# Performance work log

Hardware: AMD Instinct MI355X
Metric: run time of the kernel (lower is better)

## Reference

```python
import jax, jax.numpy as jnp
import numpy as np

N = 50000
E = 1600000
INDIM, HIDIM, OUTDIM = 256, 128, 64


def setup_inputs() -> dict:
    key = jax.random.key(0)
    ks = jax.random.split(key, 4)
    x = jax.random.normal(ks[0], (N, INDIM), dtype=jnp.float32)
    edge_index = jax.random.randint(ks[1], (2, E), 0, N, dtype=jnp.int32)
    W1 = jax.random.normal(ks[2], (INDIM, HIDIM), dtype=jnp.float32) / np.float32(np.sqrt(INDIM))
    b1 = jnp.zeros((HIDIM,), dtype=jnp.float32)
    W2 = jax.random.normal(ks[3], (HIDIM, OUTDIM), dtype=jnp.float32) / np.float32(np.sqrt(HIDIM))
    b2 = jnp.zeros((OUTDIM,), dtype=jnp.float32)
    return {"x": x, "edge_index": edge_index, "W1": W1, "b1": b1, "W2": W2, "b2": b2}


def _gcn_conv(x, row, col, norm, W, b):
    # PyG GCNConv: transform first, then normalized scatter-add aggregation, then bias
    h = x @ W                              # [N, out]
    msg = h[row] * norm[:, None]           # gather source features, scale by edge norm
    out = jax.ops.segment_sum(msg, col, num_segments=x.shape[0])  # scatter-add to dst
    return out + b


def reference(x, edge_index, W1, b1, W2, b2):
    n = x.shape[0]
    # add self loops (PyG default add_self_loops=True)
    loops = jnp.arange(n, dtype=edge_index.dtype)
    row = jnp.concatenate([edge_index[0], loops])  # source nodes
    col = jnp.concatenate([edge_index[1], loops])  # destination nodes
    # symmetric normalization: deg^{-1/2}[row] * deg^{-1/2}[col], deg over dst incl. self loops
    deg = jax.ops.segment_sum(jnp.ones_like(col, dtype=x.dtype), col, num_segments=n)
    dinv = jnp.where(deg > 0, jax.lax.rsqrt(jnp.maximum(deg, 1.0)), 0.0)
    norm = dinv[row] * dinv[col]
    h = jax.nn.relu(_gcn_conv(x, row, col, norm, W1, b1))
    return _gcn_conv(h, row, col, norm, W2, b2)
```

## Files before the change

### kernel.cpp

```cpp
#include <hip/hip_runtime.h>

#define NN 50000
#define NE 1600000
#define INDIM 256
#define HIDIM 128
#define OUTDIM 64

#define NRANGE 128
#define RSPAN 400
#define ACAP 16384
#define NBBLK 1563
#define NDEG 256

typedef unsigned int uint;
typedef unsigned long long ull;
typedef unsigned short ushort;
typedef __attribute__((ext_vector_type(8))) short bf16x8;
typedef __attribute__((ext_vector_type(4))) float f32x4;

__device__ __forceinline__ ushort f2bf(float f) {
    uint u = __float_as_uint(f);
    uint r = (u + 0x7FFFu + ((u >> 16) & 1u)) >> 16;
    return (ushort)r;
}
__device__ __forceinline__ uint pk2(float a, float b) {
    return (uint)f2bf(a) | ((uint)f2bf(b) << 16);
}
__device__ __forceinline__ float bf_lo(uint u) { return __uint_as_float(u << 16); }
__device__ __forceinline__ float bf_hi(uint u) { return __uint_as_float(u & 0xFFFF0000u); }

#define ACC8(u) do { \
    a0 += bf_lo((u).x); a1 += bf_hi((u).x); \
    a2 += bf_lo((u).y); a3 += bf_hi((u).y); \
    a4 += bf_lo((u).z); a5 += bf_hi((u).z); \
    a6 += bf_lo((u).w); a7 += bf_hi((u).w); \
} while (0)


__global__ void k_wt(const float* __restrict__ W1, const float* __restrict__ W2,
                     ushort* __restrict__ W1T, ushort* __restrict__ W2T) {
    int idx = blockIdx.x * 256 + threadIdx.x;
    if (idx < INDIM * HIDIM) {
        int k = idx / HIDIM, nn = idx % HIDIM;
        W1T[nn * INDIM + k] = f2bf(W1[idx]);
    } else {
        int j = idx - INDIM * HIDIM;
        if (j < HIDIM * OUTDIM) {
            int k = j / OUTDIM, nn = j % OUTDIM;
            W2T[nn * HIDIM + k] = f2bf(W2[j]);
        }
    }
}


__global__ void k_bcnt(const int* __restrict__ col, int* __restrict__ bcnt,
                       int* __restrict__ dhist) {
    __shared__ int bins[NRANGE];
    int tid = threadIdx.x;
    if (blockIdx.x == 0) dhist[tid] = 0;
    if (tid < NRANGE) bins[tid] = 0;
    __syncthreads();
    int base = blockIdx.x * 1024 + tid;
#pragma unroll
    for (int k = 0; k < 4; k++) {
        int i = base + k * 256;
        if (i < NE) atomicAdd(&bins[col[i] / RSPAN], 1);
    }
    __syncthreads();
    if (tid < NRANGE) bcnt[tid * NBBLK + blockIdx.x] = bins[tid];
}


__global__ void k_bscan(const int* __restrict__ bcnt, int* __restrict__ bbase,
                        int* __restrict__ rcur) {
    __shared__ int wsum[16];
    __shared__ int woff[16];
    int r = blockIdx.x;
    const int* src = bcnt + r * NBBLK;
    int* dst = bbase + r * NBBLK;
    int tid = threadIdx.x, lane = tid & 63, wid = tid >> 6;
    int seg = tid * 2;
    int l0 = (seg < NBBLK) ? src[seg] : 0;
    int l1 = (seg + 1 < NBBLK) ? src[seg + 1] : 0;
    int sum = l0 + l1;
    int incl = sum;
#pragma unroll
    for (int off = 1; off < 64; off <<= 1) {
        int t = __shfl_up(incl, off);
        if (lane >= off) incl += t;
    }
    if (lane == 63) wsum[wid] = incl;
    __syncthreads();
    if (wid == 0 && lane < 16) {
        int wv = wsum[lane];
        int wincl = wv;
#pragma unroll
        for (int off = 1; off < 16; off <<= 1) {
            int t = __shfl_up(wincl, off);
            if (lane >= off) wincl += t;
        }
        woff[lane] = wincl - wv;
    }
    __syncthreads();
    int run = incl - sum + woff[wid];
    if (seg < NBBLK) dst[seg] = run;
    if (seg + 1 < NBBLK) dst[seg + 1] = run + l0;
    if (tid == 1023) rcur[r] = run + sum;
}


__global__ void k_bscat(const int* __restrict__ row, const int* __restrict__ col,
                        const int* __restrict__ bbase, uint* __restrict__ staged) {
    __shared__ int cur[NRANGE];
    int tid = threadIdx.x;
    if (tid < NRANGE) cur[tid] = bbase[tid * NBBLK + blockIdx.x];
    __syncthreads();
    int base = blockIdx.x * 1024 + tid;
#pragma unroll
    for (int k = 0; k < 4; k++) {
        int i = base + k * 256;
        if (i < NE) {
            int d = col[i], s = row[i];
            int r = d / RSPAN;
            int off = atomicAdd(&cur[r], 1);
            staged[(size_t)r * ACAP + off] = ((uint)s << 10) | (uint)(d - r * RSPAN);
        }
    }
}


__global__ void k_sort(const uint* __restrict__ staged, const int* __restrict__ rcur,
                       int* __restrict__ row_ptr, float* __restrict__ dinv,
                       ushort* __restrict__ ssrc, int* __restrict__ dhist) {
    __shared__ int bins[RSPAN];
    __shared__ int wsum[16];
    __shared__ int woff[16];
    __shared__ int dh[NDEG];
    int r = blockIdx.x;
    int tid = threadIdx.x, lane = tid & 63, wid = tid >> 6;
    int lo = r * RSPAN;
    int count = rcur[r];
    int base = 0;
    for (int rr = 0; rr < r; rr++) base += rcur[rr];
    const uint* st = staged + (size_t)r * ACAP;

    if (tid < RSPAN) bins[tid] = 0;
    if (tid < NDEG) dh[tid] = 0;
    __syncthreads();

    for (int i = tid; i < count; i += 1024)
        atomicAdd(&bins[st[i] & 1023u], 1);
    __syncthreads();

    int v = (tid < RSPAN) ? bins[tid] : 0;
    int incl = v;
#pragma unroll
    for (int off = 1; off < 64; off <<= 1) {
        int t = __shfl_up(incl, off);
        if (lane >= off) incl += t;
    }
    if (lane == 63) wsum[wid] = incl;
    __syncthreads();
    if (wid == 0 && lane < 16) {
        int wv = wsum[lane];
        int wincl = wv;
#pragma unroll
        for (int off = 1; off < 16; off <<= 1) {
            int t = __shfl_up(wincl, off);
            if (lane >= off) wincl += t;
        }
        woff[lane] = wincl - wv;
    }
    __syncthreads();
    int excl = incl - v + woff[wid];
    int idx = lo + tid;
    if (tid < RSPAN && idx <= NN) {
        if (idx < NN) {
            row_ptr[idx] = base + excl;
            dinv[idx] = rsqrtf((float)(v + 1));
            atomicAdd(&dh[min(v, NDEG - 1)], 1);
        } else {
            row_ptr[NN] = base + excl;
        }
    }
    __syncthreads();
    if (tid < RSPAN) bins[tid] = base + excl;
    __syncthreads();
    if (tid < NDEG && dh[tid]) atomicAdd(&dhist[tid], dh[tid]);

    for (int i = tid; i < count; i += 1024) {
        uint rec = st[i];
        int pos = atomicAdd(&bins[rec & 1023u], 1);
        ssrc[pos] = (ushort)(rec >> 10);
    }
}


__global__ void k_dscan(const int* __restrict__ dhist, int* __restrict__ dstart,
                        int* __restrict__ dcur, int* __restrict__ ebase) {
    int lane = threadIdx.x;
    int b = lane * 4;
    int v0 = dhist[b], v1 = dhist[b + 1], v2 = dhist[b + 2], v3 = dhist[b + 3];
    int w0 = v0 * b, w1 = v1 * (b + 1), w2 = v2 * (b + 2), w3 = v3 * (b + 3);
    int s = v0 + v1 + v2 + v3;
    int sw = w0 + w1 + w2 + w3;
    int incl = s, inclw = sw;
#pragma unroll
    for (int off = 1; off < 64; off <<= 1) {
        int t = __shfl_up(incl, off);
        int t2 = __shfl_up(inclw, off);
        if (lane >= off) { incl += t; inclw += t2; }
    }
    int excl = incl - s, exclw = inclw - sw;
    dstart[b] = excl;            dcur[b] = excl;            ebase[b] = exclw;
    dstart[b + 1] = excl + v0;   dcur[b + 1] = excl + v0;   ebase[b + 1] = exclw + w0;
    dstart[b + 2] = excl + v0 + v1; dcur[b + 2] = excl + v0 + v1; ebase[b + 2] = exclw + w0 + w1;
    dstart[b + 3] = excl + v0 + v1 + v2; dcur[b + 3] = excl + v0 + v1 + v2; ebase[b + 3] = exclw + w0 + w1 + w2;
}


__global__ void k_dscat(const int* __restrict__ row_ptr, const float* __restrict__ dinv,
                        const int* __restrict__ dstart, int* __restrict__ dcur,
                        const int* __restrict__ ebase, int* __restrict__ perm,
                        int* __restrict__ row_ptr_p, float* __restrict__ dinv_p) {
    __shared__ int h[NDEG];
    __shared__ int boff[NDEG];
    int tid = threadIdx.x;
    int d = blockIdx.x * 256 + tid;
    h[tid] = 0;
    __syncthreads();
    int bin = 0, myoff = 0, deg = 0;
    if (d < NN) {
        deg = row_ptr[d + 1] - row_ptr[d];
        bin = min(deg, NDEG - 1);
        myoff = atomicAdd(&h[bin], 1);
    }
    __syncthreads();
    if (h[tid]) boff[tid] = atomicAdd(&dcur[tid], h[tid]);
    __syncthreads();
    if (d < NN) {
        int di = boff[bin] + myoff;
        perm[di] = d;
        int grank = di - dstart[bin];
        row_ptr_p[di] = ebase[bin] + grank * deg;
        dinv_p[di] = dinv[d];
    }
    if (d == 0) row_ptr_p[NN] = NE;
}


__global__ void k_csrperm(const int* __restrict__ perm, const int* __restrict__ row_ptr,
                          const int* __restrict__ row_ptr_p, const ushort* __restrict__ ssrc,
                          ushort* __restrict__ ssrc_p) {
    int g = blockIdx.x * 256 + threadIdx.x;
    int di = g >> 2, j = g & 3;
    if (di >= NN) return;
    int d = perm[di];
    int e0p = row_ptr_p[di];
    int deg = row_ptr_p[di + 1] - e0p;
    int e0 = row_ptr[d];
    for (int k = j; k < deg; k += 4)
        ssrc_p[e0p + k] = ssrc[e0 + k];
}


__global__ void k_gemm1(const float* __restrict__ A, const ushort* __restrict__ W1T,
                        const float* __restrict__ dinv, ushort* __restrict__ g1s, int n) {
    __shared__ ushort As[64 * 40];
    __shared__ ushort Bs[128 * 40];
    int tid = threadIdx.x;
    int w = tid >> 6, lane = tid & 63;
    int ln = lane & 15, quad = lane >> 4;
    int row0 = blockIdx.x * 64;
    int n0 = w * 32;

    f32x4 acc[4][2];
#pragma unroll
    for (int m = 0; m < 4; m++)
#pragma unroll
        for (int t = 0; t < 2; t++) acc[m][t] = (f32x4){0.f, 0.f, 0.f, 0.f};

    int ar = tid >> 2;
    int ac = (tid & 3) * 8;

    for (int k0 = 0; k0 < INDIM; k0 += 32) {
        {
            int gr = row0 + ar;
            uint4 u = make_uint4(0, 0, 0, 0);
            if (gr < n) {
                const float* p = A + (size_t)gr * INDIM + k0 + ac;
                float4 v0 = *(const float4*)p;
                float4 v1 = *(const float4*)(p + 4);
                u.x = pk2(v0.x, v0.y); u.y = pk2(v0.z, v0.w);
                u.z = pk2(v1.x, v1.y); u.w = pk2(v1.z, v1.w);
            }
            *(uint4*)(As + ar * 40 + ac) = u;
        }
#pragma unroll
        for (int it = 0; it < 2; it++) {
            int idx = tid + it * 256;
            int bn = idx >> 2, bc = (idx & 3) * 8;
            uint4 u = *(const uint4*)(W1T + (size_t)bn * INDIM + k0 + bc);
            *(uint4*)(Bs + bn * 40 + bc) = u;
        }
        __syncthreads();

        bf16x8 af[4], bf[2];
#pragma unroll
        for (int m = 0; m < 4; m++)
            af[m] = *(const bf16x8*)(As + (m * 16 + ln) * 40 + quad * 8);
#pragma unroll
        for (int t = 0; t < 2; t++)
            bf[t] = *(const bf16x8*)(Bs + (n0 + t * 16 + ln) * 40 + quad * 8);
#pragma unroll
        for (int m = 0; m < 4; m++)
#pragma unroll
            for (int t = 0; t < 2; t++)
                acc[m][t] = __builtin_amdgcn_mfma_f32_16x16x32_bf16(af[m], bf[t], acc[m][t], 0, 0, 0);
        __syncthreads();
    }

    int slice = w >> 1;
    int fbase = (w & 1) * 32;
#pragma unroll
    for (int m = 0; m < 4; m++) {
#pragma unroll
        for (int r = 0; r < 4; r++) {
            int gr = row0 + m * 16 + quad * 4 + r;
            if (gr < n) {
                float dv = dinv[gr];
#pragma unroll
                for (int t = 0; t < 2; t++) {
                    int cj = t * 16 + ln;
                    g1s[((size_t)slice * NN + gr) * 64 + fbase + cj] = f2bf(acc[m][t][r] * dv);
                }
            }
        }
    }
}


__global__ void k_agg1(const ushort* __restrict__ g1s, const float* __restrict__ dinv_p,
                       const int* __restrict__ row_ptr_p, const ushort* __restrict__ ssrc_p,
                       const int* __restrict__ perm, const float* __restrict__ b1,
                       ushort* __restrict__ hrb) {
    int slice = blockIdx.x & 1;
    int dbase = (blockIdx.x >> 1) * 32;
    int wid = threadIdx.x >> 6, lane = threadIdx.x & 63;
    int grp = lane >> 3, fl = lane & 7;
    int di = dbase + wid * 8 + grp;
    if (di >= NN) return;
    int d = perm[di];
    const ushort* gs = g1s + (size_t)slice * NN * 64 + fl * 8;
    float a0 = 0.f, a1 = 0.f, a2 = 0.f, a3 = 0.f;
    float a4 = 0.f, a5 = 0.f, a6 = 0.f, a7 = 0.f;
    int e0 = row_ptr_p[di], e1 = row_ptr_p[di + 1];
    if (e1 > e0) {
        int last = e1 - 1;
        int sB0 = ssrc_p[min(e0 + 0, last)];
        int sB1 = ssrc_p[min(e0 + 1, last)];
        int sB2 = ssrc_p[min(e0 + 2, last)];
        int sB3 = ssrc_p[min(e0 + 3, last)];
        uint4 uA0 = *(const uint4*)(gs + (size_t)sB0 * 64);
        uint4 uA1 = *(const uint4*)(gs + (size_t)sB1 * 64);
        uint4 uA2 = *(const uint4*)(gs + (size_t)sB2 * 64);
        uint4 uA3 = *(const uint4*)(gs + (size_t)sB3 * 64);
        sB0 = ssrc_p[min(e0 + 4, last)];
        sB1 = ssrc_p[min(e0 + 5, last)];
        sB2 = ssrc_p[min(e0 + 6, last)];
        sB3 = ssrc_p[min(e0 + 7, last)];
        for (int eb = e0; eb < e1; eb += 4) {
            int p0 = ssrc_p[min(eb + 8, last)];
            int p1 = ssrc_p[min(eb + 9, last)];
            int p2 = ssrc_p[min(eb + 10, last)];
            int p3 = ssrc_p[min(eb + 11, last)];
            uint4 v0 = *(const uint4*)(gs + (size_t)sB0 * 64);
            uint4 v1 = *(const uint4*)(gs + (size_t)sB1 * 64);
            uint4 v2 = *(const uint4*)(gs + (size_t)sB2 * 64);
            uint4 v3 = *(const uint4*)(gs + (size_t)sB3 * 64);
            uint4 z = make_uint4(0u, 0u, 0u, 0u);
            if (eb + 1 >= e1) uA1 = z;
            if (eb + 2 >= e1) uA2 = z;
            if (eb + 3 >= e1) uA3 = z;
            ACC8(uA0); ACC8(uA1); ACC8(uA2); ACC8(uA3);
            uA0 = v0; uA1 = v1; uA2 = v2; uA3 = v3;
            sB0 = p0; sB1 = p1; sB2 = p2; sB3 = p3;
        }
    }
    uint4 ud = *(const uint4*)(gs + (size_t)d * 64);
    ACC8(ud);
    float dv = dinv_p[di];
    const float* bp = b1 + slice * 64 + fl * 8;
    float4 bb0 = *(const float4*)bp;
    float4 bb1 = *(const float4*)(bp + 4);
    uint4 o;
    o.x = pk2(fmaxf(a0 * dv + bb0.x, 0.f), fmaxf(a1 * dv + bb0.y, 0.f));
    o.y = pk2(fmaxf(a2 * dv + bb0.z, 0.f), fmaxf(a3 * dv + bb0.w, 0.f));
    o.z = pk2(fmaxf(a4 * dv + bb1.x, 0.f), fmaxf(a5 * dv + bb1.y, 0.f));
    o.w = pk2(fmaxf(a6 * dv + bb1.z, 0.f), fmaxf(a7 * dv + bb1.w, 0.f));
    *(uint4*)(hrb + ((size_t)slice * NN + di) * 64 + fl * 8) = o;
}


__global__ void k_gemm2(const ushort* __restrict__ hrb, const ushort* __restrict__ W2T,
                        const float* __restrict__ dinv_p, const int* __restrict__ perm,
                        ushort* __restrict__ g2s, int n) {
    __shared__ ushort As[64 * 40];
    __shared__ ushort Bs[64 * 40];
    int tid = threadIdx.x;
    int w = tid >> 6, lane = tid & 63;
    int ln = lane & 15, quad = lane >> 4;
    int row0 = blockIdx.x * 64;
    int n0 = w * 16;

    f32x4 acc[4];
#pragma unroll
    for (int m = 0; m < 4; m++) acc[m] = (f32x4){0.f, 0.f, 0.f, 0.f};

    int ar = tid >> 2;
    int ac = (tid & 3) * 8;

    for (int k0 = 0; k0 < HIDIM; k0 += 32) {
        {
            int gr = row0 + ar;
            uint4 u = make_uint4(0, 0, 0, 0);
            if (gr < n) u = *(const uint4*)(hrb + ((size_t)(k0 >> 6) * NN + gr) * 64 + (k0 & 63) + ac);
            *(uint4*)(As + ar * 40 + ac) = u;
        }
        {
            int bn = tid >> 2, bc = (tid & 3) * 8;
            uint4 u = *(const uint4*)(W2T + (size_t)bn * HIDIM + k0 + bc);
            *(uint4*)(Bs + bn * 40 + bc) = u;
        }
        __syncthreads();

        bf16x8 bf = *(const bf16x8*)(Bs + (n0 + ln) * 40 + quad * 8);
#pragma unroll
        for (int m = 0; m < 4; m++) {
            bf16x8 af = *(const bf16x8*)(As + (m * 16 + ln) * 40 + quad * 8);
            acc[m] = __builtin_amdgcn_mfma_f32_16x16x32_bf16(af, bf, acc[m], 0, 0, 0);
        }
        __syncthreads();
    }

    int col = n0 + ln;
#pragma unroll
    for (int m = 0; m < 4; m++) {
#pragma unroll
        for (int r = 0; r < 4; r++) {
            int gr = row0 + m * 16 + quad * 4 + r;
            if (gr < n) {
                int gd = perm[gr];
                g2s[(size_t)gd * 64 + col] = f2bf(acc[m][r] * dinv_p[gr]);
            }
        }
    }
}


__global__ void k_agg2(const ushort* __restrict__ g2s, const float* __restrict__ dinv_p,
                       const int* __restrict__ row_ptr_p, const ushort* __restrict__ ssrc_p,
                       const int* __restrict__ perm, const float* __restrict__ b2,
                       float* __restrict__ out) {
    int dbase = blockIdx.x * 32;
    int wid = threadIdx.x >> 6, lane = threadIdx.x & 63;
    int grp = lane >> 3, fl = lane & 7;
    int di = dbase + wid * 8 + grp;
    if (di >= NN) return;
    int d = perm[di];
    const ushort* gs = g2s + fl * 8;
    float a0 = 0.f, a1 = 0.f, a2 = 0.f, a3 = 0.f;
    float a4 = 0.f, a5 = 0.f, a6 = 0.f, a7 = 0.f;
    int e0 = row_ptr_p[di], e1 = row_ptr_p[di + 1];
    if (e1 > e0) {
        int last = e1 - 1;
        int sB0 = ssrc_p[min(e0 + 0, last)];
        int sB1 = ssrc_p[min(e0 + 1, last)];
        int sB2 = ssrc_p[min(e0 + 2, last)];
        int sB3 = ssrc_p[min(e0 + 3, last)];
        uint4 uA0 = *(const uint4*)(gs + (size_t)sB0 * 64);
        uint4 uA1 = *(const uint4*)(gs + (size_t)sB1 * 64);
        uint4 uA2 = *(const uint4*)(gs + (size_t)sB2 * 64);
        uint4 uA3 = *(const uint4*)(gs + (size_t)sB3 * 64);
        sB0 = ssrc_p[min(e0 + 4, last)];
        sB1 = ssrc_p[min(e0 + 5, last)];
        sB2 = ssrc_p[min(e0 + 6, last)];
        sB3 = ssrc_p[min(e0 + 7, last)];
        for (int eb = e0; eb < e1; eb += 4) {
            int p0 = ssrc_p[min(eb + 8, last)];
            int p1 = ssrc_p[min(eb + 9, last)];
            int p2 = ssrc_p[min(eb + 10, last)];
            int p3 = ssrc_p[min(eb + 11, last)];
            uint4 v0 = *(const uint4*)(gs + (size_t)sB0 * 64);
            uint4 v1 = *(const uint4*)(gs + (size_t)sB1 * 64);
            uint4 v2 = *(const uint4*)(gs + (size_t)sB2 * 64);
            uint4 v3 = *(const uint4*)(gs + (size_t)sB3 * 64);
            uint4 z = make_uint4(0u, 0u, 0u, 0u);
            if (eb + 1 >= e1) uA1 = z;
            if (eb + 2 >= e1) uA2 = z;
            if (eb + 3 >= e1) uA3 = z;
            ACC8(uA0); ACC8(uA1); ACC8(uA2); ACC8(uA3);
            uA0 = v0; uA1 = v1; uA2 = v2; uA3 = v3;
            sB0 = p0; sB1 = p1; sB2 = p2; sB3 = p3;
        }
    }
    uint4 ud = *(const uint4*)(gs + (size_t)d * 64);
    ACC8(ud);
    float dv = dinv_p[di];
    const float* bp = b2 + fl * 8;
    float4 bb0 = *(const float4*)bp;
    float4 bb1 = *(const float4*)(bp + 4);
    float4 r0, r1;
    r0.x = a0 * dv + bb0.x;
    r0.y = a1 * dv + bb0.y;
    r0.z = a2 * dv + bb0.z;
    r0.w = a3 * dv + bb0.w;
    r1.x = a4 * dv + bb1.x;
    r1.y = a5 * dv + bb1.y;
    r1.z = a6 * dv + bb1.z;
    r1.w = a7 * dv + bb1.w;
    float* op = out + (size_t)d * OUTDIM + fl * 8;
    *(float4*)op = r0;
    *(float4*)(op + 4) = r1;
}


extern "C" void kernel_launch(void* const* d_in, const int* in_sizes, int n_in,
                              void* d_out, int out_size, void* d_ws, size_t ws_size,
                              hipStream_t stream) {
    const float* x   = (const float*)d_in[0];
    const int*   ei  = (const int*)d_in[1];
    const float* W1  = (const float*)d_in[2];
    const float* b1  = (const float*)d_in[3];
    const float* W2  = (const float*)d_in[4];
    const float* b2  = (const float*)d_in[5];
    float* out = (float*)d_out;

    const int* row = ei;
    const int* col = ei + NE;

    size_t off = 0;
    auto alloc = [&](size_t bytes) {
        void* p = (char*)d_ws + off;
        off += (bytes + 255) & ~(size_t)255;
        return p;
    };
    float*  dinv     = (float*) alloc((size_t)NN * 4);
    int*    row_ptr  = (int*)   alloc((size_t)(NN + 1) * 4);
    int*    rcur     = (int*)   alloc(NRANGE * 4);
    int*    bcnt     = (int*)   alloc((size_t)NRANGE * NBBLK * 4);
    int*    bbase    = (int*)   alloc((size_t)NRANGE * NBBLK * 4);
    uint*   staged   = (uint*)  alloc((size_t)NRANGE * ACAP * 4);
    ushort* ssrc     = (ushort*)alloc((size_t)NE * 2);
    ushort* ssrc_p   = (ushort*)alloc((size_t)NE * 2);
    ushort* W1T      = (ushort*)alloc((size_t)INDIM * HIDIM * 2);
    ushort* W2T      = (ushort*)alloc((size_t)HIDIM * OUTDIM * 2);
    ushort* g1s      = (ushort*)alloc((size_t)NN * HIDIM * 2);
    ushort* hrb      = (ushort*)alloc((size_t)NN * HIDIM * 2);
    ushort* g2s      = (ushort*)alloc((size_t)NN * OUTDIM * 2);
    int*    dhist    = (int*)   alloc((size_t)NDEG * 4);
    int*    dstart   = (int*)   alloc((size_t)NDEG * 4);
    int*    dcur     = (int*)   alloc((size_t)NDEG * 4);
    int*    ebase    = (int*)   alloc((size_t)NDEG * 4);
    int*    perm     = (int*)   alloc((size_t)NN * 4);
    int*    row_ptr_p= (int*)   alloc((size_t)(NN + 1) * 4);
    float*  dinv_p   = (float*) alloc((size_t)NN * 4);

    const int nb32 = (NN + 31) / 32;
    const int nb64 = (NN + 63) / 64;

    k_wt<<<(INDIM * HIDIM + HIDIM * OUTDIM + 255) / 256, 256, 0, stream>>>(W1, W2, W1T, W2T);

    k_bcnt<<<NBBLK, 256, 0, stream>>>(col, bcnt, dhist);
    k_bscan<<<NRANGE, 1024, 0, stream>>>(bcnt, bbase, rcur);
    k_bscat<<<NBBLK, 256, 0, stream>>>(row, col, bbase, staged);

    k_sort<<<NRANGE, 1024, 0, stream>>>(staged, rcur, row_ptr, dinv, ssrc, dhist);

    k_dscan<<<1, 64, 0, stream>>>(dhist, dstart, dcur, ebase);
    k_dscat<<<(NN + 255) / 256, 256, 0, stream>>>(row_ptr, dinv, dstart, dcur, ebase,
                                                  perm, row_ptr_p, dinv_p);
    k_csrperm<<<(NN * 4 + 255) / 256, 256, 0, stream>>>(perm, row_ptr, row_ptr_p, ssrc, ssrc_p);

    k_gemm1<<<nb64, 256, 0, stream>>>(x, W1T, dinv, g1s, NN);
    k_agg1<<<nb32 * 2, 256, 0, stream>>>(g1s, dinv_p, row_ptr_p, ssrc_p, perm, b1, hrb);
    k_gemm2<<<nb64, 256, 0, stream>>>(hrb, W2T, dinv_p, perm, g2s, NN);
    k_agg2<<<nb32, 256, 0, stream>>>(g2s, dinv_p, row_ptr_p, ssrc_p, perm, b2, out);
}
```

Baseline: 228.6 us.

## Fold degree-sort permutation into per-range sort kernel, dropping three preprocessing kernels

Each range block of k_sort now builds a local degree histogram, scans it in shared memory and ranks its 400 nodes by degree. It then writes perm, row_ptr_p and dinv_p directly and scatters sources straight into the permuted CSR. This removes k_dscan, k_dscat and k_csrperm, along with the intermediate CSR and the global dhist. The aim is to cut launch overhead and an extra pass over the edge array. The trade-off is that nodes are ordered by degree only within each 400-node range rather than globally, which may weaken load balancing in the aggregation kernels.

```diff
diff --git a/kernel.cpp b/kernel.cpp
--- a/kernel.cpp
+++ b/kernel.cpp
@@ -53,11 +53,9 @@
 }
 
 
-__global__ void k_bcnt(const int* __restrict__ col, int* __restrict__ bcnt,
-                       int* __restrict__ dhist) {
+__global__ void k_bcnt(const int* __restrict__ col, int* __restrict__ bcnt) {
     __shared__ int bins[NRANGE];
     int tid = threadIdx.x;
-    if (blockIdx.x == 0) dhist[tid] = 0;
     if (tid < NRANGE) bins[tid] = 0;
     __syncthreads();
     int base = blockIdx.x * 1024 + tid;
@@ -130,18 +128,26 @@
 
 
 __global__ void k_sort(const uint* __restrict__ staged, const int* __restrict__ rcur,
-                       int* __restrict__ row_ptr, float* __restrict__ dinv,
-                       ushort* __restrict__ ssrc, int* __restrict__ dhist) {
+                       float* __restrict__ dinv, float* __restrict__ dinv_p,
+                       int* __restrict__ row_ptr_p, int* __restrict__ perm,
+                       ushort* __restrict__ ssrc_p) {
     __shared__ int bins[RSPAN];
+    __shared__ int pdeg[RSPAN];
+    __shared__ int prow[RSPAN];
+    __shared__ int lperm[RSPAN];
+    __shared__ int dh[NDEG];
     __shared__ int wsum[16];
     __shared__ int woff[16];
-    __shared__ int dh[NDEG];
     int r = blockIdx.x;
     int tid = threadIdx.x, lane = tid & 63, wid = tid >> 6;
     int lo = r * RSPAN;
     int count = rcur[r];
-    int base = 0;
-    for (int rr = 0; rr < r; rr++) base += rcur[rr];
+    int rbase = 0;
+    for (int rr = 0; rr < r; rr++) rbase += rcur[rr];
+    if (lo >= NN) {
+        if (lo == NN && tid == 0) row_ptr_p[NN] = rbase;
+        return;
+    }
     const uint* st = staged + (size_t)r * ACAP;
 
     if (tid < RSPAN) bins[tid] = 0;
@@ -152,7 +158,38 @@
         atomicAdd(&bins[st[i] & 1023u], 1);
     __syncthreads();
 
-    int v = (tid < RSPAN) ? bins[tid] : 0;
+    int deg = (tid < RSPAN) ? bins[tid] : 0;
+    bool valid = tid < RSPAN;
+    if (valid) {
+        dinv[lo + tid] = rsqrtf((float)(deg + 1));
+        atomicAdd(&dh[min(deg, NDEG - 1)], 1);
+    }
+    __syncthreads();
+
+    if (wid == 0) {
+        int b = lane * 4;
+        int v0 = dh[b], v1 = dh[b + 1], v2 = dh[b + 2], v3 = dh[b + 3];
+        int s = v0 + v1 + v2 + v3;
+        int incl = s;
+#pragma unroll
+        for (int off = 1; off < 64; off <<= 1) {
+            int t = __shfl_up(incl, off);
+            if (lane >= off) incl += t;
+        }
+        int excl = incl - s;
+        dh[b] = excl;
+        dh[b + 1] = excl + v0;
+        dh[b + 2] = excl + v0 + v1;
+        dh[b + 3] = excl + v0 + v1 + v2;
+    }
+    __syncthreads();
+
+    int rl = 0;
+    if (valid) rl = atomicAdd(&dh[min(deg, NDEG - 1)], 1);
+    if (valid) { pdeg[rl] = deg; lperm[rl] = tid; }
+    __syncthreads();
+
+    int v = (tid < RSPAN) ? pdeg[tid] : 0;
     int incl = v;
 #pragma unroll
     for (int off = 1; off < 64; off <<= 1) {
@@ -173,94 +210,24 @@
     }
     __syncthreads();
     int excl = incl - v + woff[wid];
-    int idx = lo + tid;
-    if (tid < RSPAN && idx <= NN) {
-        if (idx < NN) {
-            row_ptr[idx] = base + excl;
-            dinv[idx] = rsqrtf((float)(v + 1));
-            atomicAdd(&dh[min(v, NDEG - 1)], 1);
-        } else {
-            row_ptr[NN] = base + excl;
-        }
-    }
-    __syncthreads();
-    if (tid < RSPAN) bins[tid] = base + excl;
-    __syncthreads();
-    if (tid < NDEG && dh[tid]) atomicAdd(&dhist[tid], dh[tid]);
+    if (tid < RSPAN) prow[tid] = excl;
+    __syncthreads();
+
+    if (tid < RSPAN) {
+        int di = lo + tid;
+        row_ptr_p[di] = rbase + prow[tid];
+        perm[di] = lo + lperm[tid];
+        dinv_p[di] = rsqrtf((float)(pdeg[tid] + 1));
+    }
+    __syncthreads();
+    if (valid) bins[tid] = rbase + prow[rl];
+    __syncthreads();
 
     for (int i = tid; i < count; i += 1024) {
         uint rec = st[i];
         int pos = atomicAdd(&bins[rec & 1023u], 1);
-        ssrc[pos] = (ushort)(rec >> 10);
-    }
-}
-
-
-__global__ void k_dscan(const int* __restrict__ dhist, int* __restrict__ dstart,
-                        int* __restrict__ dcur, int* __restrict__ ebase) {
-    int lane = threadIdx.x;
-    int b = lane * 4;
-    int v0 = dhist[b], v1 = dhist[b + 1], v2 = dhist[b + 2], v3 = dhist[b + 3];
-    int w0 = v0 * b, w1 = v1 * (b + 1), w2 = v2 * (b + 2), w3 = v3 * (b + 3);
-    int s = v0 + v1 + v2 + v3;
-    int sw = w0 + w1 + w2 + w3;
-    int incl = s, inclw = sw;
-#pragma unroll
-    for (int off = 1; off < 64; off <<= 1) {
-        int t = __shfl_up(incl, off);
-        int t2 = __shfl_up(inclw, off);
-        if (lane >= off) { incl += t; inclw += t2; }
-    }
-    int excl = incl - s, exclw = inclw - sw;
-    dstart[b] = excl;            dcur[b] = excl;            ebase[b] = exclw;
-    dstart[b + 1] = excl + v0;   dcur[b + 1] = excl + v0;   ebase[b + 1] = exclw + w0;
-    dstart[b + 2] = excl + v0 + v1; dcur[b + 2] = excl + v0 + v1; ebase[b + 2] = exclw + w0 + w1;
-    dstart[b + 3] = excl + v0 + v1 + v2; dcur[b + 3] = excl + v0 + v1 + v2; ebase[b + 3] = exclw + w0 + w1 + w2;
-}
-
-
-__global__ void k_dscat(const int* __restrict__ row_ptr, const float* __restrict__ dinv,
-                        const int* __restrict__ dstart, int* __restrict__ dcur,
-                        const int* __restrict__ ebase, int* __restrict__ perm,
-                        int* __restrict__ row_ptr_p, float* __restrict__ dinv_p) {
-    __shared__ int h[NDEG];
-    __shared__ int boff[NDEG];
-    int tid = threadIdx.x;
-    int d = blockIdx.x * 256 + tid;
-    h[tid] = 0;
-    __syncthreads();
-    int bin = 0, myoff = 0, deg = 0;
-    if (d < NN) {
-        deg = row_ptr[d + 1] - row_ptr[d];
-        bin = min(deg, NDEG - 1);
-        myoff = atomicAdd(&h[bin], 1);
-    }
-    __syncthreads();
-    if (h[tid]) boff[tid] = atomicAdd(&dcur[tid], h[tid]);
-    __syncthreads();
-    if (d < NN) {
-        int di = boff[bin] + myoff;
-        perm[di] = d;
-        int grank = di - dstart[bin];
-        row_ptr_p[di] = ebase[bin] + grank * deg;
-        dinv_p[di] = dinv[d];
-    }
-    if (d == 0) row_ptr_p[NN] = NE;
-}
-
-
-__global__ void k_csrperm(const int* __restrict__ perm, const int* __restrict__ row_ptr,
-                          const int* __restrict__ row_ptr_p, const ushort* __restrict__ ssrc,
-                          ushort* __restrict__ ssrc_p) {
-    int g = blockIdx.x * 256 + threadIdx.x;
-    int di = g >> 2, j = g & 3;
-    if (di >= NN) return;
-    int d = perm[di];
-    int e0p = row_ptr_p[di];
-    int deg = row_ptr_p[di + 1] - e0p;
-    int e0 = row_ptr[d];
-    for (int k = j; k < deg; k += 4)
-        ssrc_p[e0p + k] = ssrc[e0 + k];
+        ssrc_p[pos] = (ushort)(rec >> 10);
+    }
 }
 
 
@@ -546,22 +513,16 @@
         return p;
     };
     float*  dinv     = (float*) alloc((size_t)NN * 4);
-    int*    row_ptr  = (int*)   alloc((size_t)(NN + 1) * 4);
     int*    rcur     = (int*)   alloc(NRANGE * 4);
     int*    bcnt     = (int*)   alloc((size_t)NRANGE * NBBLK * 4);
     int*    bbase    = (int*)   alloc((size_t)NRANGE * NBBLK * 4);
     uint*   staged   = (uint*)  alloc((size_t)NRANGE * ACAP * 4);
-    ushort* ssrc     = (ushort*)alloc((size_t)NE * 2);
     ushort* ssrc_p   = (ushort*)alloc((size_t)NE * 2);
     ushort* W1T      = (ushort*)alloc((size_t)INDIM * HIDIM * 2);
     ushort* W2T      = (ushort*)alloc((size_t)HIDIM * OUTDIM * 2);
     ushort* g1s      = (ushort*)alloc((size_t)NN * HIDIM * 2);
     ushort* hrb      = (ushort*)alloc((size_t)NN * HIDIM * 2);
     ushort* g2s      = (ushort*)alloc((size_t)NN * OUTDIM * 2);
-    int*    dhist    = (int*)   alloc((size_t)NDEG * 4);
-    int*    dstart   = (int*)   alloc((size_t)NDEG * 4);
-    int*    dcur     = (int*)   alloc((size_t)NDEG * 4);
-    int*    ebase    = (int*)   alloc((size_t)NDEG * 4);
     int*    perm     = (int*)   alloc((size_t)NN * 4);
     int*    row_ptr_p= (int*)   alloc((size_t)(NN + 1) * 4);
     float*  dinv_p   = (float*) alloc((size_t)NN * 4);
@@ -571,16 +532,11 @@
 
     k_wt<<<(INDIM * HIDIM + HIDIM * OUTDIM + 255) / 256, 256, 0, stream>>>(W1, W2, W1T, W2T);
 
-    k_bcnt<<<NBBLK, 256, 0, stream>>>(col, bcnt, dhist);
+    k_bcnt<<<NBBLK, 256, 0, stream>>>(col, bcnt);
     k_bscan<<<NRANGE, 1024, 0, stream>>>(bcnt, bbase, rcur);
     k_bscat<<<NBBLK, 256, 0, stream>>>(row, col, bbase, staged);
 
-    k_sort<<<NRANGE, 1024, 0, stream>>>(staged, rcur, row_ptr, dinv, ssrc, dhist);
-
-    k_dscan<<<1, 64, 0, stream>>>(dhist, dstart, dcur, ebase);
-    k_dscat<<<(NN + 255) / 256, 256, 0, stream>>>(row_ptr, dinv, dstart, dcur, ebase,
-                                                  perm, row_ptr_p, dinv_p);
-    k_csrperm<<<(NN * 4 + 255) / 256, 256, 0, stream>>>(perm, row_ptr, row_ptr_p, ssrc, ssrc_p);
+    k_sort<<<NRANGE, 1024, 0, stream>>>(staged, rcur, dinv, dinv_p, row_ptr_p, perm, ssrc_p);
 
     k_gemm1<<<nb64, 256, 0, stream>>>(x, W1T, dinv, g1s, NN);
     k_agg1<<<nb32 * 2, 256, 0, stream>>>(g1s, dinv_p, row_ptr_p, ssrc_p, perm, b1, hrb);
```

New measurement: 217.2 us, median of 2. 5.0% less time.
